# Performance work log

Measured on AMD Instinct MI355X. Metric: run time of the kernel, lower is better.

## Reference

```python
import jax, jax.numpy as jnp
import numpy as np

IN_FEATURES = 4096
OUT_FEATURES = 4096
LORA_R = 64
LORA_ALPHA = 16
SCALING = LORA_ALPHA / LORA_R  # 0.25


def setup_inputs() -> dict:
    key = jax.random.key(0)
    k_x, k_w, k_s, k_a, k_b = jax.random.split(key, 5)
    x = jax.random.normal(k_x, (4, 2048, IN_FEATURES), dtype=jnp.float32)
    # int8 quantized base weight in [-8, 7] as in the torch buffer init
    weight_quantized = jax.random.randint(k_w, (OUT_FEATURES, IN_FEATURES), -8, 7, dtype=jnp.int8)
    weight_scale = jax.random.normal(k_s, (1,), dtype=jnp.float32)
    lora_A = jax.random.normal(k_a, (LORA_R, IN_FEATURES), dtype=jnp.float32) * 0.01
    # torch init is zeros; use small random values so the LoRA path is exercised
    lora_B = jax.random.normal(k_b, (OUT_FEATURES, LORA_R), dtype=jnp.float32) * 0.01
    return {"x": x, "weight_quantized": weight_quantized, "weight_scale": weight_scale,
            "lora_A": lora_A, "lora_B": lora_B}


def reference(x, weight_quantized, weight_scale, lora_A, lora_B):
    # 1. dequantize base weight on the fly: [out, in]
    w_dequant = weight_quantized.astype(x.dtype) * weight_scale
    # 2. base GEMM: [B, S, in] x [in, out] -> [B, S, out]
    base = jnp.einsum('bsi,oi->bso', x, w_dequant)
    # 3. LoRA low-rank update (dropout is identity in eval mode)
    lora = jnp.einsum('bsr,or->bso', jnp.einsum('bsi,ri->bsr', x, lora_A), lora_B)
    return base + lora * SCALING
```

## Files before the change

### kernel.cpp

```cpp
#include <hip/hip_runtime.h>

#define M_TOT 8192
#define K_TOT 4096
#define N_TOT 4096
#define RANK  64
#define SCALING 0.25f

typedef __bf16 bf16x8 __attribute__((ext_vector_type(8)));
typedef float floatx4 __attribute__((ext_vector_type(4)));
typedef unsigned short ushort8v __attribute__((ext_vector_type(8)));

static __device__ __forceinline__ unsigned short f32_to_bf16(float f) {
  unsigned int u = __float_as_uint(f);
  u += 0x7FFFu + ((u >> 16) & 1u);
  return (unsigned short)(u >> 16);
}

static __device__ __forceinline__ void async_ld16(const void* g, void* l) {
  __builtin_amdgcn_global_load_lds(
      (const __attribute__((address_space(1))) unsigned int*)g,
      (__attribute__((address_space(3))) unsigned int*)l, 16, 0, 0);
}

__global__ __launch_bounds__(256) void cvt_x_kernel(const float4* __restrict__ x,
                                                    ushort8v* __restrict__ xb) {
  int i = blockIdx.x * 256 + threadIdx.x;
  float4 v0 = x[2 * i];
  float4 v1 = x[2 * i + 1];
  ushort8v o;
  o[0] = f32_to_bf16(v0.x); o[1] = f32_to_bf16(v0.y);
  o[2] = f32_to_bf16(v0.z); o[3] = f32_to_bf16(v0.w);
  o[4] = f32_to_bf16(v1.x); o[5] = f32_to_bf16(v1.y);
  o[6] = f32_to_bf16(v1.z); o[7] = f32_to_bf16(v1.w);
  xb[i] = o;
}

__global__ __launch_bounds__(256) void build_weff_kernel(
    const int* __restrict__ wq, const float* __restrict__ scale_p,
    const float* __restrict__ A, const float* __restrict__ B,
    unsigned short* __restrict__ Weff) {
  __shared__ float Bs[64][65];
  __shared__ __align__(16) float As[64][64];

  const int tid = threadIdx.x;
  const int o0 = blockIdx.y * 64;
  const int k0 = blockIdx.x * 64;
  const float scale = scale_p[0];

  for (int i = tid; i < 64 * 64; i += 256) {
    int o = i >> 6, r = i & 63;
    Bs[o][r] = B[(size_t)(o0 + o) * RANK + r];
  }
  for (int i = tid; i < 64 * 64; i += 256) {
    int r = i >> 6, kk = i & 63;
    As[r][kk] = A[(size_t)r * K_TOT + k0 + kk];
  }
  __syncthreads();

  const int to = tid >> 4;
  const int tk = tid & 15;
  float acc[4][4] = {};
#pragma unroll 8
  for (int r = 0; r < RANK; ++r) {
    float bv[4];
#pragma unroll
    for (int a = 0; a < 4; ++a) bv[a] = Bs[to * 4 + a][r];
    floatx4 av = *(const floatx4*)&As[r][tk * 4];
#pragma unroll
    for (int a = 0; a < 4; ++a)
#pragma unroll
      for (int b = 0; b < 4; ++b) acc[a][b] += bv[a] * av[b];
  }
#pragma unroll
  for (int a = 0; a < 4; ++a) {
    const int o = o0 + to * 4 + a;
    const size_t base = (size_t)o * K_TOT + k0 + tk * 4;
    const int4 wv = *(const int4*)(wq + base);
    ushort4 st;
    st.x = f32_to_bf16((float)wv.x * scale + SCALING * acc[a][0]);
    st.y = f32_to_bf16((float)wv.y * scale + SCALING * acc[a][1]);
    st.z = f32_to_bf16((float)wv.z * scale + SCALING * acc[a][2]);
    st.w = f32_to_bf16((float)wv.w * scale + SCALING * acc[a][3]);
    *(ushort4*)(Weff + base) = st;
  }
}


template <int QM, int QN>
static __device__ __forceinline__ void ph_mfma(floatx4 (&acc)[8][4],
                                               const bf16x8 (&af)[4][2],
                                               const bf16x8 (&bf)[4][2]) {
#pragma unroll
  for (int ii = 0; ii < 4; ++ii)
#pragma unroll
    for (int jj = 0; jj < 2; ++jj) {
      floatx4 c = acc[QM * 4 + ii][QN * 2 + jj];
      c = __builtin_amdgcn_mfma_f32_16x16x32_bf16(af[ii][0], bf[QN * 2 + jj][0], c, 0, 0, 0);
      c = __builtin_amdgcn_mfma_f32_16x16x32_bf16(af[ii][1], bf[QN * 2 + jj][1], c, 0, 0, 0);
      acc[QM * 4 + ii][QN * 2 + jj] = c;
    }
}

__global__ __launch_bounds__(512, 2) void gemm_kernel(
    const unsigned short* __restrict__ Xb,
    const unsigned short* __restrict__ Wb,
    float* __restrict__ out) {
  __shared__ __align__(16) unsigned char smem[131072];

  const int tid = threadIdx.x;
  const int lane = tid & 63;
  const int wave = tid >> 6;
  const int wm = wave >> 2;
  const int wn = wave & 3;

  const int bid = blockIdx.x;
  const int swz = (bid & 7) * 64 + (bid >> 3);
  const int bM = (swz >> 4) * 256;
  const int bN = (swz & 15) * 256;

  const int srow = tid >> 3;
  const int scol = ((tid & 7) ^ (srow & 7)) * 8;
  const unsigned short* xs = Xb + (size_t)(bM + srow) * K_TOT + scol;
  const unsigned short* ws = Wb + (size_t)(bN + srow) * K_TOT + scol;

  const int rb = (lane & 15) * 128;
  const int c0 = (((lane >> 4) + 0) ^ (lane & 7)) * 16;
  const int c1 = (((lane >> 4) + 4) ^ (lane & 7)) * 16;
  const int aBase = wm * 16384;
  const int bBase = 32768 + (wn >> 1) * 16384 + (wn & 1) * 8192;

  floatx4 acc[8][4] = {};
  bf16x8 af[4][2], bf[4][2];

#define BAR() asm volatile("s_barrier" ::: "memory")
#define WAIT_LGKM0() asm volatile("s_waitcnt lgkmcnt(0)" ::: "memory")
#define WAIT_VM(N) asm volatile("s_waitcnt vmcnt(" #N ")" ::: "memory")
#define STAGE_A(BUF, H, S, KO)                                              \
  async_ld16(xs + (size_t)((H) * 128 + (S) * 64) * K_TOT + (KO),            \
             smem + (BUF) * 65536 + (H) * 16384 + (S) * 8192 + tid * 16)
#define STAGE_B(BUF, H, S, KO)                                              \
  async_ld16(ws + (size_t)((H) * 128 + (S) * 64) * K_TOT + (KO),            \
             smem + (BUF) * 65536 + 32768 + (H) * 16384 + (S) * 8192 + tid * 16)
#define DSR_A(BUF, QM, II, KS)                                              \
  af[II][KS] = *(const bf16x8*)(smem + (BUF) * 65536 + aBase +              \
                                ((QM) * 4 + (II)) * 2048 + rb + ((KS) ? c1 : c0))
#define DSR_B(BUF, J, KS)                                                   \
  bf[J][KS] = *(const bf16x8*)(smem + (BUF) * 65536 + bBase +               \
                               (J) * 2048 + rb + ((KS) ? c1 : c0))

#define GROUP(BUF, KA, KB)                                                  \
  {                                                                         \
          \
    DSR_B(BUF, 0, 0); DSR_B(BUF, 0, 1);                                     \
    DSR_B(BUF, 1, 0); DSR_B(BUF, 1, 1);                                     \
    DSR_A(BUF, 0, 0, 0); DSR_A(BUF, 0, 0, 1);                               \
    DSR_A(BUF, 0, 1, 0); DSR_A(BUF, 0, 1, 1);                               \
    DSR_A(BUF, 0, 2, 0); DSR_A(BUF, 0, 2, 1);                               \
    DSR_A(BUF, 0, 3, 0); DSR_A(BUF, 0, 3, 1);                               \
    STAGE_A((BUF) ^ 1, 0, 0, KA); STAGE_A((BUF) ^ 1, 0, 1, KA);             \
    __builtin_amdgcn_s_setprio(1);                                          \
    ph_mfma<0, 0>(acc, af, bf);                                             \
    __builtin_amdgcn_s_setprio(0);                                          \
    WAIT_LGKM0(); BAR();                                                    \
                            \
    DSR_B(BUF, 2, 0); DSR_B(BUF, 2, 1);                                     \
    DSR_B(BUF, 3, 0); DSR_B(BUF, 3, 1);                                     \
    STAGE_A((BUF) ^ 1, 1, 0, KA); STAGE_A((BUF) ^ 1, 1, 1, KA);             \
    __builtin_amdgcn_s_setprio(1);                                          \
    ph_mfma<0, 1>(acc, af, bf);                                             \
    __builtin_amdgcn_s_setprio(0);                                          \
    WAIT_LGKM0(); BAR();                                                    \
                            \
    DSR_A(BUF, 1, 0, 0); DSR_A(BUF, 1, 0, 1);                               \
    DSR_A(BUF, 1, 1, 0); DSR_A(BUF, 1, 1, 1);                               \
    DSR_A(BUF, 1, 2, 0); DSR_A(BUF, 1, 2, 1);                               \
    DSR_A(BUF, 1, 3, 0); DSR_A(BUF, 1, 3, 1);                               \
    STAGE_B(BUF, 0, 0, KB); STAGE_B(BUF, 0, 1, KB);                         \
    __builtin_amdgcn_s_setprio(1);                                          \
    ph_mfma<1, 1>(acc, af, bf);                                             \
    __builtin_amdgcn_s_setprio(0);                                          \
    WAIT_LGKM0(); BAR();                                                    \
          \
    STAGE_B(BUF, 1, 0, KB); STAGE_B(BUF, 1, 1, KB);                         \
    __builtin_amdgcn_s_setprio(1);                                          \
    ph_mfma<1, 0>(acc, af, bf);                                             \
    __builtin_amdgcn_s_setprio(0);                                          \
    WAIT_VM(4);                                                             \
    BAR();                                                                  \
  }

  STAGE_A(0, 0, 0, 0); STAGE_A(0, 0, 1, 0);
  STAGE_A(0, 1, 0, 0); STAGE_A(0, 1, 1, 0);
  STAGE_B(0, 0, 0, 0); STAGE_B(0, 0, 1, 0);
  STAGE_B(0, 1, 0, 0); STAGE_B(0, 1, 1, 0);
  STAGE_B(1, 0, 0, 64); STAGE_B(1, 0, 1, 64);
  STAGE_B(1, 1, 0, 64); STAGE_B(1, 1, 1, 64);
  WAIT_VM(0);
  BAR();

  for (int kt = 0; kt < 64; kt += 2) {
    const int ka0 = ((kt + 1) & 63) * 64;
    const int kb0 = ((kt + 2) & 63) * 64;
    const int ka1 = ((kt + 2) & 63) * 64;
    const int kb1 = ((kt + 3) & 63) * 64;
    GROUP(0, ka0, kb0);
    GROUP(1, ka1, kb1);
  }
  WAIT_VM(0);

  const int row0 = bM + wm * 128 + ((lane >> 4) << 2);
  const int col0 = bN + wn * 64 + (lane & 15);
#pragma unroll
  for (int i = 0; i < 8; ++i) {
#pragma unroll
    for (int j = 0; j < 4; ++j) {
#pragma unroll
      for (int r = 0; r < 4; ++r) {
        out[(size_t)(row0 + i * 16 + r) * N_TOT + (col0 + j * 16)] = acc[i][j][r];
      }
    }
  }
#undef BAR
#undef WAIT_LGKM0
#undef WAIT_VM
#undef STAGE_A
#undef STAGE_B
#undef DSR_A
#undef DSR_B
#undef GROUP
}

extern "C" void kernel_launch(void* const* d_in, const int* in_sizes, int n_in,
                              void* d_out, int out_size, void* d_ws, size_t ws_size,
                              hipStream_t stream) {
  const float* x      = (const float*)d_in[0];
  const int*   wq     = (const int*)d_in[1];
  const float* wscale = (const float*)d_in[2];
  const float* lora_A = (const float*)d_in[3];
  const float* lora_B = (const float*)d_in[4];
  float* out = (float*)d_out;

  unsigned short* xb   = (unsigned short*)d_ws;
  unsigned short* weff = (unsigned short*)((char*)d_ws + (size_t)M_TOT * K_TOT * 2);

  cvt_x_kernel<<<16384, 256, 0, stream>>>((const float4*)x, (ushort8v*)xb);
  build_weff_kernel<<<dim3(K_TOT / 64, N_TOT / 64), 256, 0, stream>>>(
      wq, wscale, lora_A, lora_B, weff);
  gemm_kernel<<<512, 512, 0, stream>>>(xb, weff, out);
}
```

Before: 544.3 us.

## Switch GEMM to 32x32x16 MFMA tiles and enlarge build_weff tiles

The main GEMM moves from 16x16x32 bf16 MFMA to 32x32x16 MFMA. It uses a 4x2 grid of 32x32 accumulators per wave with new LDS read offsets and a new epilogue mapping. This is meant to cut LDS fragment reads per FLOP and instruction overhead, at the cost of a different register and bank-conflict profile. The weight-building kernel also now computes 128x128 tiles with 8x8 outer products per thread, using vectorised B transpose and A loads, to reduce launch count and improve reuse.

```diff
diff --git a/kernel.cpp b/kernel.cpp
--- a/kernel.cpp
+++ b/kernel.cpp
@@ -8,6 +8,7 @@
 
 typedef __bf16 bf16x8 __attribute__((ext_vector_type(8)));
 typedef float floatx4 __attribute__((ext_vector_type(4)));
+typedef float floatx16 __attribute__((ext_vector_type(16)));
 typedef unsigned short ushort8v __attribute__((ext_vector_type(8)));
 
 static __device__ __forceinline__ unsigned short f32_to_bf16(float f) {
@@ -39,66 +40,69 @@
     const int* __restrict__ wq, const float* __restrict__ scale_p,
     const float* __restrict__ A, const float* __restrict__ B,
     unsigned short* __restrict__ Weff) {
-  __shared__ float Bs[64][65];
-  __shared__ __align__(16) float As[64][64];
+  __shared__ __align__(16) float Bts[64][128];
+  __shared__ __align__(16) float As_[64][128];
 
   const int tid = threadIdx.x;
-  const int o0 = blockIdx.y * 64;
-  const int k0 = blockIdx.x * 64;
+  const int bo = blockIdx.y * 128;
+  const int bk = blockIdx.x * 128;
   const float scale = scale_p[0];
 
-  for (int i = tid; i < 64 * 64; i += 256) {
-    int o = i >> 6, r = i & 63;
-    Bs[o][r] = B[(size_t)(o0 + o) * RANK + r];
-  }
-  for (int i = tid; i < 64 * 64; i += 256) {
-    int r = i >> 6, kk = i & 63;
-    As[r][kk] = A[(size_t)r * K_TOT + k0 + kk];
+  {
+    const int o = tid >> 1;
+    const int rh = (tid & 1) * 32;
+    const float* gb = B + (size_t)(bo + o) * RANK + rh;
+#pragma unroll
+    for (int j = 0; j < 8; ++j) {
+      float4 v = *(const float4*)(gb + j * 4);
+      Bts[rh + j * 4 + 0][o] = v.x;
+      Bts[rh + j * 4 + 1][o] = v.y;
+      Bts[rh + j * 4 + 2][o] = v.z;
+      Bts[rh + j * 4 + 3][o] = v.w;
+    }
+  }
+#pragma unroll
+  for (int j = 0; j < 8; ++j) {
+    const int ii = j * 1024 + tid * 4;
+    const int r = ii >> 7, c = ii & 127;
+    *(floatx4*)&As_[r][c] = *(const floatx4*)(A + (size_t)r * K_TOT + bk + c);
   }
   __syncthreads();
 
   const int to = tid >> 4;
   const int tk = tid & 15;
-  float acc[4][4] = {};
-#pragma unroll 8
+  float acc[8][8] = {};
+#pragma unroll 4
   for (int r = 0; r < RANK; ++r) {
-    float bv[4];
-#pragma unroll
-    for (int a = 0; a < 4; ++a) bv[a] = Bs[to * 4 + a][r];
-    floatx4 av = *(const floatx4*)&As[r][tk * 4];
-#pragma unroll
-    for (int a = 0; a < 4; ++a)
-#pragma unroll
-      for (int b = 0; b < 4; ++b) acc[a][b] += bv[a] * av[b];
-  }
-#pragma unroll
-  for (int a = 0; a < 4; ++a) {
-    const int o = o0 + to * 4 + a;
-    const size_t base = (size_t)o * K_TOT + k0 + tk * 4;
-    const int4 wv = *(const int4*)(wq + base);
-    ushort4 st;
-    st.x = f32_to_bf16((float)wv.x * scale + SCALING * acc[a][0]);
-    st.y = f32_to_bf16((float)wv.y * scale + SCALING * acc[a][1]);
-    st.z = f32_to_bf16((float)wv.z * scale + SCALING * acc[a][2]);
-    st.w = f32_to_bf16((float)wv.w * scale + SCALING * acc[a][3]);
-    *(ushort4*)(Weff + base) = st;
-  }
-}
-
-
-template <int QM, int QN>
-static __device__ __forceinline__ void ph_mfma(floatx4 (&acc)[8][4],
-                                               const bf16x8 (&af)[4][2],
-                                               const bf16x8 (&bf)[4][2]) {
-#pragma unroll
-  for (int ii = 0; ii < 4; ++ii)
-#pragma unroll
-    for (int jj = 0; jj < 2; ++jj) {
-      floatx4 c = acc[QM * 4 + ii][QN * 2 + jj];
-      c = __builtin_amdgcn_mfma_f32_16x16x32_bf16(af[ii][0], bf[QN * 2 + jj][0], c, 0, 0, 0);
-      c = __builtin_amdgcn_mfma_f32_16x16x32_bf16(af[ii][1], bf[QN * 2 + jj][1], c, 0, 0, 0);
-      acc[QM * 4 + ii][QN * 2 + jj] = c;
-    }
+    floatx4 b0 = *(const floatx4*)&Bts[r][to * 8];
+    floatx4 b1 = *(const floatx4*)&Bts[r][to * 8 + 4];
+    floatx4 a0 = *(const floatx4*)&As_[r][tk * 8];
+    floatx4 a1 = *(const floatx4*)&As_[r][tk * 8 + 4];
+    float bv[8] = {b0.x, b0.y, b0.z, b0.w, b1.x, b1.y, b1.z, b1.w};
+    float av[8] = {a0.x, a0.y, a0.z, a0.w, a1.x, a1.y, a1.z, a1.w};
+#pragma unroll
+    for (int a = 0; a < 8; ++a)
+#pragma unroll
+      for (int b = 0; b < 8; ++b) acc[a][b] += bv[a] * av[b];
+  }
+
+#pragma unroll
+  for (int a = 0; a < 8; ++a) {
+    const int o = bo + to * 8 + a;
+    const size_t base = (size_t)o * K_TOT + bk + tk * 8;
+    const int4 w0 = *(const int4*)(wq + base);
+    const int4 w1 = *(const int4*)(wq + base + 4);
+    ushort8v st;
+    st[0] = f32_to_bf16((float)w0.x * scale + SCALING * acc[a][0]);
+    st[1] = f32_to_bf16((float)w0.y * scale + SCALING * acc[a][1]);
+    st[2] = f32_to_bf16((float)w0.z * scale + SCALING * acc[a][2]);
+    st[3] = f32_to_bf16((float)w0.w * scale + SCALING * acc[a][3]);
+    st[4] = f32_to_bf16((float)w1.x * scale + SCALING * acc[a][4]);
+    st[5] = f32_to_bf16((float)w1.y * scale + SCALING * acc[a][5]);
+    st[6] = f32_to_bf16((float)w1.z * scale + SCALING * acc[a][6]);
+    st[7] = f32_to_bf16((float)w1.w * scale + SCALING * acc[a][7]);
+    *(ushort8v*)(Weff + base) = st;
+  }
 }
 
 __global__ __launch_bounds__(512, 2) void gemm_kernel(
@@ -123,14 +127,19 @@
   const unsigned short* xs = Xb + (size_t)(bM + srow) * K_TOT + scol;
   const unsigned short* ws = Wb + (size_t)(bN + srow) * K_TOT + scol;
 
-  const int rb = (lane & 15) * 128;
-  const int c0 = (((lane >> 4) + 0) ^ (lane & 7)) * 16;
-  const int c1 = (((lane >> 4) + 4) ^ (lane & 7)) * 16;
+  const int hi = lane >> 5;
+  const int l7 = lane & 7;
+  const int rb = (lane & 31) * 128;
+  const int cc0 = ((0 * 2 + hi) ^ l7) * 16;
+  const int cc1 = ((1 * 2 + hi) ^ l7) * 16;
+  const int cc2 = ((2 * 2 + hi) ^ l7) * 16;
+  const int cc3 = ((3 * 2 + hi) ^ l7) * 16;
   const int aBase = wm * 16384;
-  const int bBase = 32768 + (wn >> 1) * 16384 + (wn & 1) * 8192;
-
-  floatx4 acc[8][4] = {};
-  bf16x8 af[4][2], bf[4][2];
+  const int bBase = 32768 + wn * 8192;
+
+  floatx16 acc[4][2] = {};
+  bf16x8 af[2][2];
+  bf16x8 bf[2][4];
 
 #define BAR() asm volatile("s_barrier" ::: "memory")
 #define WAIT_LGKM0() asm volatile("s_waitcnt lgkmcnt(0)" ::: "memory")
@@ -141,49 +150,56 @@
 #define STAGE_B(BUF, H, S, KO)                                              \
   async_ld16(ws + (size_t)((H) * 128 + (S) * 64) * K_TOT + (KO),            \
              smem + (BUF) * 65536 + 32768 + (H) * 16384 + (S) * 8192 + tid * 16)
-#define DSR_A(BUF, QM, II, KS)                                              \
-  af[II][KS] = *(const bf16x8*)(smem + (BUF) * 65536 + aBase +              \
-                                ((QM) * 4 + (II)) * 2048 + rb + ((KS) ? c1 : c0))
-#define DSR_B(BUF, J, KS)                                                   \
-  bf[J][KS] = *(const bf16x8*)(smem + (BUF) * 65536 + bBase +               \
-                               (J) * 2048 + rb + ((KS) ? c1 : c0))
+#define RD_A(BUF, MI, MM, KK, CC)                                           \
+  af[MM][KK] = *(const bf16x8*)(smem + (BUF) * 65536 + aBase + (MI) * 4096 + rb + (CC))
+#define RD_B(BUF, NJ, KS, CC)                                               \
+  bf[NJ][KS] = *(const bf16x8*)(smem + (BUF) * 65536 + bBase + (NJ) * 4096 + rb + (CC))
+
+#define MFMA_OCT(MB, PB)                                                    \
+  {                                                                         \
+    _Pragma("unroll") for (int kk = 0; kk < 2; ++kk)                        \
+    _Pragma("unroll") for (int mm = 0; mm < 2; ++mm)                        \
+    _Pragma("unroll") for (int nn = 0; nn < 2; ++nn)                        \
+      acc[(MB) + mm][nn] = __builtin_amdgcn_mfma_f32_32x32x16_bf16(         \
+          af[mm][kk], bf[nn][kk + (PB)], acc[(MB) + mm][nn], 0, 0, 0);      \
+  }
 
 #define GROUP(BUF, KA, KB)                                                  \
   {                                                                         \
-          \
-    DSR_B(BUF, 0, 0); DSR_B(BUF, 0, 1);                                     \
-    DSR_B(BUF, 1, 0); DSR_B(BUF, 1, 1);                                     \
-    DSR_A(BUF, 0, 0, 0); DSR_A(BUF, 0, 0, 1);                               \
-    DSR_A(BUF, 0, 1, 0); DSR_A(BUF, 0, 1, 1);                               \
-    DSR_A(BUF, 0, 2, 0); DSR_A(BUF, 0, 2, 1);                               \
-    DSR_A(BUF, 0, 3, 0); DSR_A(BUF, 0, 3, 1);                               \
+                            \
+    RD_B(BUF, 0, 0, cc0); RD_B(BUF, 1, 0, cc0);                             \
+    RD_A(BUF, 0, 0, 0, cc0); RD_A(BUF, 1, 1, 0, cc0);                       \
+    RD_B(BUF, 0, 1, cc1); RD_B(BUF, 1, 1, cc1);                             \
+    RD_A(BUF, 0, 0, 1, cc1); RD_A(BUF, 1, 1, 1, cc1);                       \
     STAGE_A((BUF) ^ 1, 0, 0, KA); STAGE_A((BUF) ^ 1, 0, 1, KA);             \
     __builtin_amdgcn_s_setprio(1);                                          \
-    ph_mfma<0, 0>(acc, af, bf);                                             \
+    MFMA_OCT(0, 0);                                                         \
     __builtin_amdgcn_s_setprio(0);                                          \
     WAIT_LGKM0(); BAR();                                                    \
                             \
-    DSR_B(BUF, 2, 0); DSR_B(BUF, 2, 1);                                     \
-    DSR_B(BUF, 3, 0); DSR_B(BUF, 3, 1);                                     \
+    RD_B(BUF, 0, 2, cc2); RD_B(BUF, 1, 2, cc2);                             \
+    RD_A(BUF, 0, 0, 0, cc2); RD_A(BUF, 1, 1, 0, cc2);                       \
+    RD_B(BUF, 0, 3, cc3); RD_B(BUF, 1, 3, cc3);                             \
+    RD_A(BUF, 0, 0, 1, cc3); RD_A(BUF, 1, 1, 1, cc3);                       \
     STAGE_A((BUF) ^ 1, 1, 0, KA); STAGE_A((BUF) ^ 1, 1, 1, KA);             \
     __builtin_amdgcn_s_setprio(1);                                          \
-    ph_mfma<0, 1>(acc, af, bf);                                             \
+    MFMA_OCT(0, 2);                                                         \
     __builtin_amdgcn_s_setprio(0);                                          \
     WAIT_LGKM0(); BAR();                                                    \
-                            \
-    DSR_A(BUF, 1, 0, 0); DSR_A(BUF, 1, 0, 1);                               \
-    DSR_A(BUF, 1, 1, 0); DSR_A(BUF, 1, 1, 1);                               \
-    DSR_A(BUF, 1, 2, 0); DSR_A(BUF, 1, 2, 1);                               \
-    DSR_A(BUF, 1, 3, 0); DSR_A(BUF, 1, 3, 1);                               \
+     \
+    RD_A(BUF, 2, 0, 0, cc0); RD_A(BUF, 3, 1, 0, cc0);                       \
+    RD_A(BUF, 2, 0, 1, cc1); RD_A(BUF, 3, 1, 1, cc1);                       \
     STAGE_B(BUF, 0, 0, KB); STAGE_B(BUF, 0, 1, KB);                         \
     __builtin_amdgcn_s_setprio(1);                                          \
-    ph_mfma<1, 1>(acc, af, bf);                                             \
+    MFMA_OCT(2, 0);                                                         \
     __builtin_amdgcn_s_setprio(0);                                          \
     WAIT_LGKM0(); BAR();                                                    \
-          \
+                 \
+    RD_A(BUF, 2, 0, 0, cc2); RD_A(BUF, 3, 1, 0, cc2);                       \
+    RD_A(BUF, 2, 0, 1, cc3); RD_A(BUF, 3, 1, 1, cc3);                       \
     STAGE_B(BUF, 1, 0, KB); STAGE_B(BUF, 1, 1, KB);                         \
     __builtin_amdgcn_s_setprio(1);                                          \
-    ph_mfma<1, 0>(acc, af, bf);                                             \
+    MFMA_OCT(2, 2);                                                         \
     __builtin_amdgcn_s_setprio(0);                                          \
     WAIT_VM(4);                                                             \
     BAR();                                                                  \
@@ -208,16 +224,18 @@
   }
   WAIT_VM(0);
 
-  const int row0 = bM + wm * 128 + ((lane >> 4) << 2);
-  const int col0 = bN + wn * 64 + (lane & 15);
-#pragma unroll
-  for (int i = 0; i < 8; ++i) {
-#pragma unroll
-    for (int j = 0; j < 4; ++j) {
-#pragma unroll
-      for (int r = 0; r < 4; ++r) {
-        out[(size_t)(row0 + i * 16 + r) * N_TOT + (col0 + j * 16)] = acc[i][j][r];
-      }
+  const int col0 = bN + wn * 64 + (lane & 31);
+#pragma unroll
+  for (int mi = 0; mi < 4; ++mi) {
+    const int rbase = bM + wm * 128 + mi * 32 + hi * 4;
+#pragma unroll
+    for (int nj = 0; nj < 2; ++nj) {
+#pragma unroll
+      for (int rg = 0; rg < 4; ++rg)
+#pragma unroll
+        for (int rr = 0; rr < 4; ++rr)
+          out[(size_t)(rbase + rg * 8 + rr) * N_TOT + (col0 + nj * 32)] =
+              acc[mi][nj][rg * 4 + rr];
     }
   }
 #undef BAR
@@ -225,8 +243,9 @@
 #undef WAIT_VM
 #undef STAGE_A
 #undef STAGE_B
-#undef DSR_A
-#undef DSR_B
+#undef RD_A
+#undef RD_B
+#undef MFMA_OCT
 #undef GROUP
 }
 
@@ -244,7 +263,7 @@
   unsigned short* weff = (unsigned short*)((char*)d_ws + (size_t)M_TOT * K_TOT * 2);
 
   cvt_x_kernel<<<16384, 256, 0, stream>>>((const float4*)x, (ushort8v*)xb);
-  build_weff_kernel<<<dim3(K_TOT / 64, N_TOT / 64), 256, 0, stream>>>(
+  build_weff_kernel<<<dim3(K_TOT / 128, N_TOT / 128), 256, 0, stream>>>(
       wq, wscale, lora_A, lora_B, weff);
   gemm_kernel<<<512, 512, 0, stream>>>(xb, weff, out);
 }
```

Result: faster. 525.9 us (-3.4%).
